# Kernel optimization log

Hardware: AMD Instinct MI355X
Metric: run time of the kernel (lower is better)

Reference implementation:

```python
import jax, jax.numpy as jnp
import numpy as np

B, T, C = 4, 2048, 1024
T_REF = 512
H = 16
D = C // H


def setup_inputs() -> dict:
    key = jax.random.key(0)
    ks = jax.random.split(key, 16)
    s = 0.02
    return {
        "x": jax.random.normal(ks[0], (B, T, C), jnp.float32),
        "ref_feat": jax.random.normal(ks[1], (B, T_REF, C), jnp.float32),
        "Wq": jax.random.normal(ks[2], (C, C), jnp.float32) * s,
        "bq": jax.random.normal(ks[3], (C,), jnp.float32) * s,
        "Wk": jax.random.normal(ks[4], (C, C), jnp.float32) * s,
        "bk": jax.random.normal(ks[5], (C,), jnp.float32) * s,
        "Wv": jax.random.normal(ks[6], (C, C), jnp.float32) * s,
        "bv": jax.random.normal(ks[7], (C,), jnp.float32) * s,
        "Wrk": jax.random.normal(ks[8], (C, C), jnp.float32) * s,
        "brk": jax.random.normal(ks[9], (C,), jnp.float32) * s,
        "Wrv": jax.random.normal(ks[10], (C, C), jnp.float32) * s,
        "brv": jax.random.normal(ks[11], (C,), jnp.float32) * s,
        "Wp": jax.random.normal(ks[12], (C, C), jnp.float32) * s,
        "bp": jax.random.normal(ks[13], (C,), jnp.float32) * s,
    }


def _heads(y):
    # [B, T, C] -> [B, H, T, D]
    b, t, c = y.shape
    return y.reshape(b, t, H, D).transpose(0, 2, 1, 3)


def reference(x, ref_feat, Wq, bq, Wk, bk, Wv, bv, Wrk, brk, Wrv, brv, Wp, bp):
    b, t, c = x.shape
    t_ref = ref_feat.shape[1]
    q = _heads(x @ Wq + bq)                      # [B,H,T,D]
    k = _heads(x @ Wk + bk)                      # [B,H,T,D]
    v = _heads(x @ Wv + bv)
    ref_k = _heads(ref_feat @ Wrk + brk)         # [B,H,Tref,D]
    ref_v = _heads(ref_feat @ Wrv + brv)
    k = jnp.concatenate([k, ref_k], axis=2)      # [B,H,T+Tref,D]
    v = jnp.concatenate([v, ref_v], axis=2)

    # additive bias: causal over self keys, fully visible over ref keys
    causal = jnp.tril(jnp.ones((t, t), dtype=bool))
    full_mask = jnp.concatenate([causal, jnp.ones((t, t_ref), dtype=bool)], axis=1)
    bias = jnp.where(full_mask, 0.0, -jnp.inf).astype(x.dtype)  # [T, T+Tref]

    scale = 1.0 / jnp.sqrt(jnp.asarray(D, x.dtype))
    scores = jnp.einsum("bhtd,bhsd->bhts", q, k) * scale + bias
    attn = jax.nn.softmax(scores, axis=-1)
    y = jnp.einsum("bhts,bhsd->bhtd", attn, v)   # [B,H,T,D]
    y = y.transpose(0, 2, 1, 3).reshape(b, t, c)
    return y @ Wp + bp
```

## Files before the change

### kernel.cpp

```cpp
#include <hip/hip_runtime.h>
#include <hip/hip_bf16.h>

typedef short s16x4 __attribute__((ext_vector_type(4)));
typedef short s16x8 __attribute__((ext_vector_type(8)));
typedef __bf16 bf16x8 __attribute__((ext_vector_type(8)));
typedef float f32x4 __attribute__((ext_vector_type(4)));
typedef float f32x16 __attribute__((ext_vector_type(16)));

#define DEVI static __device__ __forceinline__
#define QSCALE 0.18033688011112042f

DEVI unsigned short f2bf(float x) {
  union { float f; unsigned u; } a; a.f = x;
  unsigned r = a.u + 0x7fffu + ((a.u >> 16) & 1u);
  return (unsigned short)(r >> 16);
}
DEVI bf16x8 asbf(s16x8 v) {
  union { s16x8 s; bf16x8 b; } u; u.s = v; return u.b;
}
DEVI unsigned cvtpk(float lo, float hi) {
  unsigned r;
  asm("v_cvt_pk_bf16_f32 %0, %1, %2" : "=v"(r) : "v"(lo), "v"(hi));
  return r;
}
DEVI void gload16(const void* g, void* l) {
  __builtin_amdgcn_global_load_lds(
      (const __attribute__((address_space(1))) void*)g,
      (__attribute__((address_space(3))) void*)l, 16, 0, 0);
}

struct PrepArgs {
  const float* x; const float* ref; unsigned short* xg;
  const float* w[6]; unsigned short* o[6];
};

__global__ __launch_bounds__(256)
void prep(PrepArgs a) {
  __shared__ short tile[64][65];
  const int bid = blockIdx.x, t = threadIdx.x;
  if (bid < 5120) {
    int f = bid * 256 + t;
    int row = f >> 7, c8 = f & 127;
    const float* src = (row < 8192 ? a.x + (size_t)row * 1024
                                   : a.ref + (size_t)(row - 8192) * 1024) + c8 * 8;
    float4 v0 = *(const float4*)src;
    float4 v1 = *(const float4*)(src + 4);
    s16x8 o;
    o[0] = (short)f2bf(v0.x); o[1] = (short)f2bf(v0.y);
    o[2] = (short)f2bf(v0.z); o[3] = (short)f2bf(v0.w);
    o[4] = (short)f2bf(v1.x); o[5] = (short)f2bf(v1.y);
    o[6] = (short)f2bf(v1.z); o[7] = (short)f2bf(v1.w);
    int cs = (c8 & ~7) | ((c8 ^ row) & 7);
    *(s16x8*)(a.xg + (size_t)row * 1024 + cs * 8) = o;
  } else {
    int q = bid - 5120;
    int z = q >> 8, b2 = q & 255;
    const float* __restrict__ W = a.w[z];
    unsigned short* __restrict__ WT = a.o[z];
    const float sc = (z == 0) ? QSCALE : 1.0f;
    const int n0 = (b2 & 15) * 64;
    const int k0 = (b2 >> 4) * 64;
#pragma unroll
    for (int i = 0; i < 4; i++) {
      int f = t + i * 256;
      int r = f >> 4, c = (f & 15) * 4;
      float4 v = *(const float4*)(W + (size_t)(k0 + r) * 1024 + n0 + c);
      tile[r][c + 0] = (short)f2bf(v.x * sc);
      tile[r][c + 1] = (short)f2bf(v.y * sc);
      tile[r][c + 2] = (short)f2bf(v.z * sc);
      tile[r][c + 3] = (short)f2bf(v.w * sc);
    }
    __syncthreads();
#pragma unroll
    for (int i = 0; i < 2; i++) {
      int f = t + i * 256;
      int r = f >> 3, c8 = f & 7;
      s16x8 o;
#pragma unroll
      for (int jj = 0; jj < 8; jj++) o[jj] = tile[c8 * 8 + jj][r];
      *(s16x8*)(WT + (size_t)(n0 + r) * 1024 + k0 + ((c8 ^ (r & 7)) & 7) * 8) = o;
    }
  }
}

template<int MODE>
__global__ __launch_bounds__(256, 4)
void gemm_bt(const unsigned short* __restrict__ A, const unsigned short* __restrict__ BT,
             const float* __restrict__ b0, const float* __restrict__ b1,
             const float* __restrict__ b2,
             void* __restrict__ o0, void* __restrict__ o1, void* __restrict__ o2)
{
  const int K = 1024;
  __shared__ __align__(16) short As[128][64];
  __shared__ __align__(16) short Bs[128][64];
  const int t = threadIdx.x;
  const int lane = t & 63, wid = t >> 6;
  const int wm = wid >> 1, wn = wid & 1;
  const int lr = lane & 15, lg = lane >> 4;

  int nIdx, mIdx;
  if (MODE == 0) {
    int xcd = blockIdx.x & 7, r = blockIdx.x >> 3;
    mIdx = xcd * 8 + (r & 7);
    nIdx = r >> 3;
  } else {
    nIdx = blockIdx.x; mIdx = blockIdx.y;
  }
  const size_t m0 = (size_t)mIdx * 128;
  const int n0 = nIdx * 128;

  f32x4 acc[4][4];
#pragma unroll
  for (int i = 0; i < 4; i++)
#pragma unroll
    for (int j = 0; j < 4; j++) acc[i][j] = (f32x4){0.f, 0.f, 0.f, 0.f};

  const unsigned short* Abase = A + m0 * K;
  const unsigned short* Bbase = BT + (size_t)n0 * K;
  const int r_ld = t >> 3, cb_ld = t & 7;

  for (int k0 = 0; k0 < K; k0 += 64) {
#pragma unroll
    for (int i = 0; i < 4; i++) {
      int r = r_ld + i * 32;
      gload16(Abase + (size_t)r * K + k0 + cb_ld * 8,
              (short*)As + (i * 256 + wid * 64) * 8);
      gload16(Bbase + (size_t)r * K + k0 + cb_ld * 8,
              (short*)Bs + (i * 256 + wid * 64) * 8);
    }
    __syncthreads();
#pragma unroll
    for (int ks = 0; ks < 2; ks++) {
      s16x8 af[4], bfr[4];
#pragma unroll
      for (int i = 0; i < 4; i++)
        af[i] = *(const s16x8*)&As[wm * 64 + i * 16 + lr][(((ks * 4 + lg) ^ lr) & 7) * 8];
#pragma unroll
      for (int i = 0; i < 4; i++)
        bfr[i] = *(const s16x8*)&Bs[wn * 64 + i * 16 + lr][(((ks * 4 + lg) ^ lr) & 7) * 8];
#pragma unroll
      for (int mi = 0; mi < 4; mi++)
#pragma unroll
        for (int ni = 0; ni < 4; ni++)
          acc[mi][ni] = __builtin_amdgcn_mfma_f32_16x16x32_bf16(
              asbf(af[mi]), asbf(bfr[ni]), acc[mi][ni], 0, 0, 0);
    }
    __syncthreads();
  }

  const int seg = n0 >> 10;
  const float* bb = (seg == 0) ? b0 : (seg == 1 ? b1 : b2);
#pragma unroll
  for (int mi = 0; mi < 4; mi++) {
#pragma unroll
    for (int ni = 0; ni < 4; ni++) {
      int cg = n0 + wn * 64 + ni * 16 + lr;
      int c = cg & 1023;
      float bv = bb[c];
      if (MODE == 0 && seg == 0) bv *= QSCALE;
      const bool vseg = (MODE == 0 && seg == 2) || (MODE == 1 && seg == 1);
      if (MODE != 2 && vseg) {
        int rm0 = (int)m0 + wm * 64 + mi * 16 + lg * 4;
        int d = c & 63, hh = c >> 6;
        int bb_, s;
        if (MODE == 0) { bb_ = rm0 >> 11; s = rm0 & 2047; }
        else           { bb_ = rm0 >> 9;  s = 2048 + (rm0 & 511); }
        int scol = (s & ~63) + ((((s >> 3) ^ d) & 7) << 3) + (s & 7);
        unsigned short* dst = (unsigned short*)(MODE == 0 ? o2 : o1);
        short4 pk4;
        pk4.x = (short)f2bf(acc[mi][ni][0] + bv);
        pk4.y = (short)f2bf(acc[mi][ni][1] + bv);
        pk4.z = (short)f2bf(acc[mi][ni][2] + bv);
        pk4.w = (short)f2bf(acc[mi][ni][3] + bv);
        *(short4*)(dst + ((size_t)(bb_ * 16 + hh) * 64 + d) * 2560 + scol) = pk4;
      } else {
#pragma unroll
        for (int r = 0; r < 4; r++) {
          int rm = (int)m0 + wm * 64 + mi * 16 + lg * 4 + r;
          float val = acc[mi][ni][r] + bv;
          if (MODE == 2) {
            ((float*)o0)[(size_t)rm * 1024 + cg] = val;
          } else {
            size_t orow; unsigned short* dst; bool swz;
            if (MODE == 0) {
              if (seg == 0) { dst = (unsigned short*)o0; orow = rm; swz = false; }
              else { orow = (size_t)(rm >> 11) * 2560 + (rm & 2047);
                     dst = (unsigned short*)o1; swz = true; }
            } else {
              orow = (size_t)(rm >> 9) * 2560 + 2048 + (rm & 511);
              dst = (unsigned short*)o0; swz = true;
            }
            int cc = c;
            if (swz) cc = (c & ~63) | ((((c >> 3) ^ (int)orow) & 7) << 3) | (c & 7);
            dst[orow * 1024 + cc] = f2bf(val);
          }
        }
      }
    }
  }
}

__global__ __launch_bounds__(256, 4)
void attn(const unsigned short* __restrict__ Q, const unsigned short* __restrict__ Kb,
          const unsigned short* __restrict__ VbT, unsigned short* __restrict__ Y)
{
  const int T = 2048, S = 2560, C = 1024, TREF = 512;
  __shared__ __align__(16) short Ks[2][64][64];
  __shared__ __align__(16) short Vt[2][64][64];
  const int t = threadIdx.x;
  const int lane = t & 63, wid = t >> 6;
  const int l31 = lane & 31, hi = lane >> 5;
  const int j = wid >> 1, sub = wid & 1;

  const int bid = blockIdx.x;
  const int xcd = bid & 7, idx = bid >> 3;
  const int bh = xcd * 8 + (idx >> 4);
  const int bx = idx & 15;
  const int b = bh >> 4;
  const int hc = (bh & 15) * 64;
  const int qtile = j ? (31 - bx) : bx;

  const int nself = 32 - bx;
  const int ntiles = nself + TREF / 64;
  const int tdiag = j ? (nself - 1) : bx;

  auto s0_of = [&](int ti2) {
    return (ti2 < nself) ? ti2 * 64 : T + (ti2 - nself) * 64;
  };
  const int r_ld = t >> 3, cb_ld = t & 7;
  auto load_K = [&](int ti2, int buf) {
    int s0 = s0_of(ti2);
    const unsigned short* Krow = Kb + (size_t)(b * S + s0) * C + hc;
#pragma unroll
    for (int i = 0; i < 2; i++)
      gload16(Krow + (size_t)(r_ld + i * 32) * C + cb_ld * 8,
              (short*)&Ks[buf][0][0] + (i * 256 + wid * 64) * 8);
  };
  auto load_V = [&](int ti2, int buf) {
    int s0 = s0_of(ti2);
    const unsigned short* Vr = VbT + (size_t)bh * 64 * S + s0;
#pragma unroll
    for (int i = 0; i < 2; i++)
      gload16(Vr + (size_t)(r_ld + i * 32) * S + cb_ld * 8,
              (short*)&Vt[buf][0][0] + (i * 256 + wid * 64) * 8);
  };

  load_K(0, 0);
  load_V(0, 0);

  s16x8 qf[4];
  {
    size_t qrow = (size_t)(b * T + qtile * 64 + sub * 32 + l31);
#pragma unroll
    for (int ks = 0; ks < 4; ks++)
      qf[ks] = *(const s16x8*)(Q + qrow * C + hc + ks * 16 + hi * 8);
  }

  float lsum = 0.f;
  f32x16 o0 = 0.f, o1 = 0.f;

  __syncthreads();

  const int swz = (l31 & 7);

  for (int ti = 0; ti < ntiles; ti++) {
    const int cur = ti & 1;
    const bool more = (ti + 1 < ntiles);
    if (more) { load_K(ti + 1, cur ^ 1); load_V(ti + 1, cur ^ 1); }

    const bool active = j || (ti <= bx) || (ti >= nself);
    if (active) {
      f32x16 sa0 = 0.f, sa1 = 0.f;
      __builtin_amdgcn_s_setprio(1);
#pragma unroll
      for (int ks = 0; ks < 4; ks++) {
        int cb = ks * 2 + hi;
        s16x8 kf0 = *(const s16x8*)&Ks[cur][l31][((cb ^ swz) & 7) * 8];
        s16x8 kf1 = *(const s16x8*)&Ks[cur][32 + l31][((cb ^ swz) & 7) * 8];
        sa0 = __builtin_amdgcn_mfma_f32_32x32x16_bf16(
            asbf(kf0), asbf(qf[ks]), sa0, 0, 0, 0);
        sa1 = __builtin_amdgcn_mfma_f32_32x32x16_bf16(
            asbf(kf1), asbf(qf[ks]), sa1, 0, 0, 0);
      }
      __builtin_amdgcn_s_setprio(0);

      if (ti == tdiag) {
        int qg = sub * 32 + l31;
#pragma unroll
        for (int r = 0; r < 16; r++) {
          int sl = (r & 3) + 8 * (r >> 2) + 4 * hi;
          if (sl > qg)      sa0[r] = -1e30f;
          if (32 + sl > qg) sa1[r] = -1e30f;
        }
      }

#pragma unroll
      for (int r = 0; r < 16; r++) {
        sa0[r] = __builtin_amdgcn_exp2f(sa0[r]);
        sa1[r] = __builtin_amdgcn_exp2f(sa1[r]);
      }
      float sm[8];
#pragma unroll
      for (int r = 0; r < 8; r++)
        sm[r] = (sa0[2 * r] + sa0[2 * r + 1]) + (sa1[2 * r] + sa1[2 * r + 1]);
      lsum += ((sm[0] + sm[1]) + (sm[2] + sm[3])) +
              ((sm[4] + sm[5]) + (sm[6] + sm[7]));

      s16x8 pb[4];
#pragma unroll
      for (int sb = 0; sb < 2; sb++) {
        unsigned A[8];
#pragma unroll
        for (int m = 0; m < 8; m++)
          A[m] = (sb == 0) ? cvtpk(sa0[2 * m], sa0[2 * m + 1])
                           : cvtpk(sa1[2 * m], sa1[2 * m + 1]);
        {
          unsigned x0 = A[0], y0 = A[2], x1 = A[1], y1 = A[3];
          asm("v_permlane32_swap_b32 %0, %1" : "+v"(x0), "+v"(y0));
          asm("v_permlane32_swap_b32 %0, %1" : "+v"(x1), "+v"(y1));
          union { unsigned w[4]; s16x8 v; } U;
          U.w[0] = x0; U.w[1] = x1; U.w[2] = y0; U.w[3] = y1;
          pb[sb * 2] = U.v;
        }
        {
          unsigned x0 = A[4], y0 = A[6], x1 = A[5], y1 = A[7];
          asm("v_permlane32_swap_b32 %0, %1" : "+v"(x0), "+v"(y0));
          asm("v_permlane32_swap_b32 %0, %1" : "+v"(x1), "+v"(y1));
          union { unsigned w[4]; s16x8 v; } U;
          U.w[0] = x0; U.w[1] = x1; U.w[2] = y0; U.w[3] = y1;
          pb[sb * 2 + 1] = U.v;
        }
      }

      __builtin_amdgcn_s_setprio(1);
#pragma unroll
      for (int sl = 0; sl < 4; sl++) {
        int cb = sl * 2 + hi;
        s16x8 vf0 = *(const s16x8*)&Vt[cur][l31][((cb ^ swz) & 7) * 8];
        s16x8 vf1 = *(const s16x8*)&Vt[cur][32 + l31][((cb ^ swz) & 7) * 8];
        o0 = __builtin_amdgcn_mfma_f32_32x32x16_bf16(
            asbf(vf0), asbf(pb[sl]), o0, 0, 0, 0);
        o1 = __builtin_amdgcn_mfma_f32_32x32x16_bf16(
            asbf(vf1), asbf(pb[sl]), o1, 0, 0, 0);
      }
      __builtin_amdgcn_s_setprio(0);
    }

    __syncthreads();
  }

  float tot = lsum + __shfl_xor(lsum, 32, 64);
  float inv = 1.0f / tot;
  int qrow = b * T + qtile * 64 + sub * 32 + l31;
#pragma unroll
  for (int dblk = 0; dblk < 2; dblk++) {
#pragma unroll
    for (int g = 0; g < 4; g++) {
      int d = dblk * 32 + 8 * g + 4 * hi;
      float v0 = (dblk ? o1[4 * g + 0] : o0[4 * g + 0]) * inv;
      float v1 = (dblk ? o1[4 * g + 1] : o0[4 * g + 1]) * inv;
      float v2 = (dblk ? o1[4 * g + 2] : o0[4 * g + 2]) * inv;
      float v3 = (dblk ? o1[4 * g + 3] : o0[4 * g + 3]) * inv;
      short4 s4;
      s4.x = (short)f2bf(v0); s4.y = (short)f2bf(v1);
      s4.z = (short)f2bf(v2); s4.w = (short)f2bf(v3);
      int col = hc + d;
      int cb = col >> 3;
      int cs = (cb & ~7) | ((cb ^ qrow) & 7);
      *(short4*)(Y + (size_t)qrow * C + cs * 8 + (d & 7)) = s4;
    }
  }
}

extern "C" void kernel_launch(void* const* d_in, const int* in_sizes, int n_in,
                              void* d_out, int out_size, void* d_ws, size_t ws_size,
                              hipStream_t stream) {
  const float* x   = (const float*)d_in[0];
  const float* ref = (const float*)d_in[1];
  const float* Wq  = (const float*)d_in[2];
  const float* bq  = (const float*)d_in[3];
  const float* Wk  = (const float*)d_in[4];
  const float* bk  = (const float*)d_in[5];
  const float* Wv  = (const float*)d_in[6];
  const float* bv  = (const float*)d_in[7];
  const float* Wrk = (const float*)d_in[8];
  const float* brk = (const float*)d_in[9];
  const float* Wrv = (const float*)d_in[10];
  const float* brv = (const float*)d_in[11];
  const float* Wp  = (const float*)d_in[12];
  const float* bp  = (const float*)d_in[13];
  float* out = (float*)d_out;

  char* ws = (char*)d_ws;
  auto alloc = [&](size_t bytes) {
    char* p = ws; ws += (bytes + 255) & ~(size_t)255; return p;
  };
  const size_t WB = (size_t)1024 * 1024 * 2;
  unsigned short* Wall = (unsigned short*)alloc(5 * WB);
  unsigned short* WpT  = (unsigned short*)alloc(WB);
  unsigned short* xg  = (unsigned short*)alloc((size_t)10240 * 1024 * 2);
  unsigned short* rg  = xg + (size_t)8192 * 1024;
  unsigned short* qb  = (unsigned short*)alloc((size_t)8192 * 1024 * 2);
  unsigned short* kb  = (unsigned short*)alloc((size_t)4 * 2560 * 1024 * 2);
  unsigned short* vbT = (unsigned short*)alloc((size_t)4096 * 2560 * 2);
  unsigned short* yb  = (unsigned short*)alloc((size_t)8192 * 1024 * 2);

  dim3 tb(256);

  PrepArgs pa;
  pa.x = x; pa.ref = ref; pa.xg = xg;
  pa.w[0] = Wq;  pa.o[0] = Wall;
  pa.w[1] = Wk;  pa.o[1] = Wall + (size_t)1024 * 1024;
  pa.w[2] = Wv;  pa.o[2] = Wall + (size_t)2048 * 1024;
  pa.w[3] = Wrk; pa.o[3] = Wall + (size_t)3072 * 1024;
  pa.w[4] = Wrv; pa.o[4] = Wall + (size_t)4096 * 1024;
  pa.w[5] = Wp;  pa.o[5] = WpT;
  prep<<<dim3(6656), tb, 0, stream>>>(pa);

  gemm_bt<0><<<dim3(1536), tb, 0, stream>>>(xg, Wall, bq, bk, bv, qb, kb, vbT);
  gemm_bt<1><<<dim3(16, 16), tb, 0, stream>>>(rg, Wall + (size_t)3072 * 1024,
                                              brk, brv, nullptr, kb, vbT, nullptr);

  attn<<<dim3(1024), tb, 0, stream>>>(qb, kb, vbT, yb);

  gemm_bt<2><<<dim3(8, 64), tb, 0, stream>>>(yb, WpT, bp, bp, bp, out, out, out);
}
```

Measured before the change: 190.6 us.

## Split attention key tiles across wave pairs and launch one block per query tile

Previously each block handled two paired query tiles, one per wave pair, to balance causal work. Now each block handles a single query tile, and its two wave pairs split each 64-key tile into 32-key halves. Partial outputs and row sums are combined through shared memory at the end. The grid doubles to 2048 blocks, ordered so the longest tiles launch first. This cuts per-wave latency and removes the idle waves on skipped tiles, but adds a final reduction and gives each wave less MFMA work per barrier.

```diff
diff --git a/kernel.cpp b/kernel.cpp
--- a/kernel.cpp
+++ b/kernel.cpp
@@ -210,22 +210,19 @@
   const int t = threadIdx.x;
   const int lane = t & 63, wid = t >> 6;
   const int l31 = lane & 31, hi = lane >> 5;
-  const int j = wid >> 1, sub = wid & 1;
+  const int sub = wid & 1, sh = wid >> 1;
 
   const int bid = blockIdx.x;
   const int xcd = bid & 7, idx = bid >> 3;
-  const int bh = xcd * 8 + (idx >> 4);
-  const int bx = idx & 15;
+  const int bh = xcd * 8 + (idx & 7);
+  const int bx = 31 - (idx >> 3);
   const int b = bh >> 4;
   const int hc = (bh & 15) * 64;
-  const int qtile = j ? (31 - bx) : bx;
-
-  const int nself = 32 - bx;
-  const int ntiles = nself + TREF / 64;
-  const int tdiag = j ? (nself - 1) : bx;
+
+  const int ntiles = bx + 1 + TREF / 64;
 
   auto s0_of = [&](int ti2) {
-    return (ti2 < nself) ? ti2 * 64 : T + (ti2 - nself) * 64;
+    return (ti2 <= bx) ? ti2 * 64 : T + (ti2 - bx - 1) * 64;
   };
   const int r_ld = t >> 3, cb_ld = t & 7;
   auto load_K = [&](int ti2, int buf) {
@@ -250,7 +247,7 @@
 
   s16x8 qf[4];
   {
-    size_t qrow = (size_t)(b * T + qtile * 64 + sub * 32 + l31);
+    size_t qrow = (size_t)(b * T + bx * 64 + sub * 32 + l31);
 #pragma unroll
     for (int ks = 0; ks < 4; ks++)
       qf[ks] = *(const s16x8*)(Q + qrow * C + hc + ks * 16 + hi * 8);
@@ -268,106 +265,114 @@
     const bool more = (ti + 1 < ntiles);
     if (more) { load_K(ti + 1, cur ^ 1); load_V(ti + 1, cur ^ 1); }
 
-    const bool active = j || (ti <= bx) || (ti >= nself);
-    if (active) {
-      f32x16 sa0 = 0.f, sa1 = 0.f;
-      __builtin_amdgcn_s_setprio(1);
-#pragma unroll
-      for (int ks = 0; ks < 4; ks++) {
-        int cb = ks * 2 + hi;
-        s16x8 kf0 = *(const s16x8*)&Ks[cur][l31][((cb ^ swz) & 7) * 8];
-        s16x8 kf1 = *(const s16x8*)&Ks[cur][32 + l31][((cb ^ swz) & 7) * 8];
-        sa0 = __builtin_amdgcn_mfma_f32_32x32x16_bf16(
-            asbf(kf0), asbf(qf[ks]), sa0, 0, 0, 0);
-        sa1 = __builtin_amdgcn_mfma_f32_32x32x16_bf16(
-            asbf(kf1), asbf(qf[ks]), sa1, 0, 0, 0);
+    f32x16 sa = 0.f;
+    __builtin_amdgcn_s_setprio(1);
+#pragma unroll
+    for (int ks = 0; ks < 4; ks++) {
+      int cb = ks * 2 + hi;
+      s16x8 kf = *(const s16x8*)&Ks[cur][sh * 32 + l31][((cb ^ swz) & 7) * 8];
+      sa = __builtin_amdgcn_mfma_f32_32x32x16_bf16(
+          asbf(kf), asbf(qf[ks]), sa, 0, 0, 0);
+    }
+    __builtin_amdgcn_s_setprio(0);
+
+    if (ti == bx) {
+      int qg = sub * 32 + l31;
+#pragma unroll
+      for (int r = 0; r < 16; r++) {
+        int sl = sh * 32 + (r & 3) + 8 * (r >> 2) + 4 * hi;
+        if (sl > qg) sa[r] = -1e30f;
       }
-      __builtin_amdgcn_s_setprio(0);
-
-      if (ti == tdiag) {
-        int qg = sub * 32 + l31;
-#pragma unroll
-        for (int r = 0; r < 16; r++) {
-          int sl = (r & 3) + 8 * (r >> 2) + 4 * hi;
-          if (sl > qg)      sa0[r] = -1e30f;
-          if (32 + sl > qg) sa1[r] = -1e30f;
+    }
+
+#pragma unroll
+    for (int r = 0; r < 16; r++) sa[r] = __builtin_amdgcn_exp2f(sa[r]);
+    float sm[4];
+#pragma unroll
+    for (int r = 0; r < 4; r++)
+      sm[r] = (sa[4 * r] + sa[4 * r + 1]) + (sa[4 * r + 2] + sa[4 * r + 3]);
+    lsum += (sm[0] + sm[1]) + (sm[2] + sm[3]);
+
+    unsigned A[8];
+#pragma unroll
+    for (int m = 0; m < 8; m++) A[m] = cvtpk(sa[2 * m], sa[2 * m + 1]);
+    s16x8 pb[2];
+    {
+      unsigned x0 = A[0], y0 = A[2], x1 = A[1], y1 = A[3];
+      asm("v_permlane32_swap_b32 %0, %1" : "+v"(x0), "+v"(y0));
+      asm("v_permlane32_swap_b32 %0, %1" : "+v"(x1), "+v"(y1));
+      union { unsigned w[4]; s16x8 v; } U;
+      U.w[0] = x0; U.w[1] = x1; U.w[2] = y0; U.w[3] = y1;
+      pb[0] = U.v;
+    }
+    {
+      unsigned x0 = A[4], y0 = A[6], x1 = A[5], y1 = A[7];
+      asm("v_permlane32_swap_b32 %0, %1" : "+v"(x0), "+v"(y0));
+      asm("v_permlane32_swap_b32 %0, %1" : "+v"(x1), "+v"(y1));
+      union { unsigned w[4]; s16x8 v; } U;
+      U.w[0] = x0; U.w[1] = x1; U.w[2] = y0; U.w[3] = y1;
+      pb[1] = U.v;
+    }
+
+    __builtin_amdgcn_s_setprio(1);
+#pragma unroll
+    for (int sl = 0; sl < 2; sl++) {
+      int cb = sh * 4 + sl * 2 + hi;
+      s16x8 vf0 = *(const s16x8*)&Vt[cur][l31][((cb ^ swz) & 7) * 8];
+      s16x8 vf1 = *(const s16x8*)&Vt[cur][32 + l31][((cb ^ swz) & 7) * 8];
+      o0 = __builtin_amdgcn_mfma_f32_32x32x16_bf16(
+          asbf(vf0), asbf(pb[sl]), o0, 0, 0, 0);
+      o1 = __builtin_amdgcn_mfma_f32_32x32x16_bf16(
+          asbf(vf1), asbf(pb[sl]), o1, 0, 0, 0);
+    }
+    __builtin_amdgcn_s_setprio(0);
+
+    __syncthreads();
+  }
+
+  float ls2 = lsum + __shfl_xor(lsum, 32, 64);
+  float* red = (float*)&Ks[0][0][0];
+  float* lred = (float*)&Vt[0][0][0];
+  if (sh == 1) {
+#pragma unroll
+    for (int dblk = 0; dblk < 2; dblk++)
+#pragma unroll
+      for (int g = 0; g < 4; g++)
+#pragma unroll
+        for (int r = 0; r < 4; r++) {
+          int d = dblk * 32 + 8 * g + 4 * hi + r;
+          red[(sub * 32 + l31) * 64 + (d ^ l31)] =
+              dblk ? o1[4 * g + r] : o0[4 * g + r];
         }
+    if (hi == 0) lred[sub * 32 + l31] = ls2;
+  }
+  __syncthreads();
+  if (sh == 0) {
+    float tot = ls2 + lred[sub * 32 + l31];
+    float inv = 1.0f / tot;
+    int base = (sub * 32 + l31) * 64;
+    int qrow = b * T + bx * 64 + sub * 32 + l31;
+#pragma unroll
+    for (int dblk = 0; dblk < 2; dblk++) {
+#pragma unroll
+      for (int g = 0; g < 4; g++) {
+        int d0 = dblk * 32 + 8 * g + 4 * hi;
+        float v0 = ((dblk ? o1[4 * g + 0] : o0[4 * g + 0]) +
+                    red[base + ((d0 + 0) ^ l31)]) * inv;
+        float v1 = ((dblk ? o1[4 * g + 1] : o0[4 * g + 1]) +
+                    red[base + ((d0 + 1) ^ l31)]) * inv;
+        float v2 = ((dblk ? o1[4 * g + 2] : o0[4 * g + 2]) +
+                    red[base + ((d0 + 2) ^ l31)]) * inv;
+        float v3 = ((dblk ? o1[4 * g + 3] : o0[4 * g + 3]) +
+                    red[base + ((d0 + 3) ^ l31)]) * inv;
+        short4 s4;
+        s4.x = (short)f2bf(v0); s4.y = (short)f2bf(v1);
+        s4.z = (short)f2bf(v2); s4.w = (short)f2bf(v3);
+        int col = hc + d0;
+        int cb = col >> 3;
+        int cs = (cb & ~7) | ((cb ^ qrow) & 7);
+        *(short4*)(Y + (size_t)qrow * C + cs * 8 + (d0 & 7)) = s4;
       }
-
-#pragma unroll
-      for (int r = 0; r < 16; r++) {
-        sa0[r] = __builtin_amdgcn_exp2f(sa0[r]);
-        sa1[r] = __builtin_amdgcn_exp2f(sa1[r]);
-      }
-      float sm[8];
-#pragma unroll
-      for (int r = 0; r < 8; r++)
-        sm[r] = (sa0[2 * r] + sa0[2 * r + 1]) + (sa1[2 * r] + sa1[2 * r + 1]);
-      lsum += ((sm[0] + sm[1]) + (sm[2] + sm[3])) +
-              ((sm[4] + sm[5]) + (sm[6] + sm[7]));
-
-      s16x8 pb[4];
-#pragma unroll
-      for (int sb = 0; sb < 2; sb++) {
-        unsigned A[8];
-#pragma unroll
-        for (int m = 0; m < 8; m++)
-          A[m] = (sb == 0) ? cvtpk(sa0[2 * m], sa0[2 * m + 1])
-                           : cvtpk(sa1[2 * m], sa1[2 * m + 1]);
-        {
-          unsigned x0 = A[0], y0 = A[2], x1 = A[1], y1 = A[3];
-          asm("v_permlane32_swap_b32 %0, %1" : "+v"(x0), "+v"(y0));
-          asm("v_permlane32_swap_b32 %0, %1" : "+v"(x1), "+v"(y1));
-          union { unsigned w[4]; s16x8 v; } U;
-          U.w[0] = x0; U.w[1] = x1; U.w[2] = y0; U.w[3] = y1;
-          pb[sb * 2] = U.v;
-        }
-        {
-          unsigned x0 = A[4], y0 = A[6], x1 = A[5], y1 = A[7];
-          asm("v_permlane32_swap_b32 %0, %1" : "+v"(x0), "+v"(y0));
-          asm("v_permlane32_swap_b32 %0, %1" : "+v"(x1), "+v"(y1));
-          union { unsigned w[4]; s16x8 v; } U;
-          U.w[0] = x0; U.w[1] = x1; U.w[2] = y0; U.w[3] = y1;
-          pb[sb * 2 + 1] = U.v;
-        }
-      }
-
-      __builtin_amdgcn_s_setprio(1);
-#pragma unroll
-      for (int sl = 0; sl < 4; sl++) {
-        int cb = sl * 2 + hi;
-        s16x8 vf0 = *(const s16x8*)&Vt[cur][l31][((cb ^ swz) & 7) * 8];
-        s16x8 vf1 = *(const s16x8*)&Vt[cur][32 + l31][((cb ^ swz) & 7) * 8];
-        o0 = __builtin_amdgcn_mfma_f32_32x32x16_bf16(
-            asbf(vf0), asbf(pb[sl]), o0, 0, 0, 0);
-        o1 = __builtin_amdgcn_mfma_f32_32x32x16_bf16(
-            asbf(vf1), asbf(pb[sl]), o1, 0, 0, 0);
-      }
-      __builtin_amdgcn_s_setprio(0);
-    }
-
-    __syncthreads();
-  }
-
-  float tot = lsum + __shfl_xor(lsum, 32, 64);
-  float inv = 1.0f / tot;
-  int qrow = b * T + qtile * 64 + sub * 32 + l31;
-#pragma unroll
-  for (int dblk = 0; dblk < 2; dblk++) {
-#pragma unroll
-    for (int g = 0; g < 4; g++) {
-      int d = dblk * 32 + 8 * g + 4 * hi;
-      float v0 = (dblk ? o1[4 * g + 0] : o0[4 * g + 0]) * inv;
-      float v1 = (dblk ? o1[4 * g + 1] : o0[4 * g + 1]) * inv;
-      float v2 = (dblk ? o1[4 * g + 2] : o0[4 * g + 2]) * inv;
-      float v3 = (dblk ? o1[4 * g + 3] : o0[4 * g + 3]) * inv;
-      short4 s4;
-      s4.x = (short)f2bf(v0); s4.y = (short)f2bf(v1);
-      s4.z = (short)f2bf(v2); s4.w = (short)f2bf(v3);
-      int col = hc + d;
-      int cb = col >> 3;
-      int cs = (cb & ~7) | ((cb ^ qrow) & 7);
-      *(short4*)(Y + (size_t)qrow * C + cs * 8 + (d & 7)) = s4;
     }
   }
 }
@@ -421,7 +426,7 @@
   gemm_bt<1><<<dim3(16, 16), tb, 0, stream>>>(rg, Wall + (size_t)3072 * 1024,
                                               brk, brv, nullptr, kb, vbT, nullptr);
 
-  attn<<<dim3(1024), tb, 0, stream>>>(qb, kb, vbT, yb);
+  attn<<<dim3(2048), tb, 0, stream>>>(qb, kb, vbT, yb);
 
   gemm_bt<2><<<dim3(8, 64), tb, 0, stream>>>(yb, WpT, bp, bp, bp, out, out, out);
 }
```

Measured after the change: 189.7 us. About the same (-0.5%).
